# Kernel optimization log

Measured on AMD Instinct MI355X. Metric: run time of the kernel, lower is better.

Reference implementation:

```python
import jax, jax.numpy as jnp
import numpy as np

B = 262144
HID = 256
HEADS = 8


def setup_inputs() -> dict:
    key = jax.random.key(0)
    ks = jax.random.split(key, 8)
    s = 1.0 / np.sqrt(HID)
    return {
        "fine_messages": jax.random.normal(ks[0], (B, HID), jnp.float32),
        "coarse_messages": jax.random.normal(ks[1], (B, HID), jnp.float32),
        "motif_features": jax.random.normal(ks[2], (B, HID), jnp.float32),
        "Wq": jax.random.normal(ks[3], (HID, HID), jnp.float32) * s,
        "Wk": jax.random.normal(ks[4], (HID, HID), jnp.float32) * s,
        "Wv": jax.random.normal(ks[5], (HID, HID), jnp.float32) * s,
        "Wo": jax.random.normal(ks[6], (HID, HID), jnp.float32) * s,
        "bo": jax.random.normal(ks[7], (HID,), jnp.float32) * s,
        "heads": HEADS,
    }


def reference(fine_messages, coarse_messages, motif_features, Wq, Wk, Wv, Wo, bo, heads):
    b, hid = motif_features.shape
    d_k = hid // heads
    # K/V share the same pre-projection input: [fine; coarse] -> (B, 2, hid)
    kv_in = jnp.stack([fine_messages, coarse_messages], axis=1)
    # torch Linear(x) = x @ W.T (no bias on q/k/v projections)
    q = (motif_features @ Wq.T).reshape(b, heads, d_k)          # (B, H, d_k) single query
    k = (kv_in @ Wk.T).reshape(b, 2, heads, d_k)                # (B, 2, H, d_k)
    v = (kv_in @ Wv.T).reshape(b, 2, heads, d_k)
    # NOTE: original divides by d_k, not sqrt(d_k)
    scores = jnp.einsum("bhd,bshd->bhs", q, k) / d_k            # (B, H, 2)
    att = jax.nn.softmax(scores, axis=-1)
    out = jnp.einsum("bhs,bshd->bhd", att, v).reshape(b, hid)   # (B, hid)
    return out @ Wo.T + bo
```

## Files before the change

kernel.cpp:

```cpp
#include <hip/hip_runtime.h>

#define B_TOT 262144
#define HID   256
#define NHEAD 8
#define BR    64
#define NTHR  256

typedef __bf16 bf16_t;
typedef __attribute__((ext_vector_type(8))) __bf16 bf16x8;
typedef __attribute__((ext_vector_type(4))) float  f32x4;


#define PHASE_SYNC(N)                                                  \
  do {                                                                 \
    asm volatile("s_waitcnt vmcnt(" #N ") lgkmcnt(0)" ::: "memory");   \
    __builtin_amdgcn_s_barrier();                                      \
  } while (0)

static __device__ __forceinline__ f32x4 mfma16(bf16x8 a, bf16x8 b, f32x4 c) {
  return __builtin_amdgcn_mfma_f32_16x16x32_bf16(a, b, c, 0, 0, 0);
}

static __device__ __forceinline__ bf16x8 cvt8(float4 a, float4 b) {
  bf16x8 r;
  r[0] = (bf16_t)a.x; r[1] = (bf16_t)a.y; r[2] = (bf16_t)a.z; r[3] = (bf16_t)a.w;
  r[4] = (bf16_t)b.x; r[5] = (bf16_t)b.y; r[6] = (bf16_t)b.z; r[7] = (bf16_t)b.w;
  return r;
}

static __device__ __forceinline__ bf16x8 pin8(bf16x8 v) {
  f32x4 t = __builtin_bit_cast(f32x4, v);
  asm volatile("" : "+v"(t));
  return __builtin_bit_cast(bf16x8, t);
}

typedef __attribute__((address_space(3))) void lds_void;
typedef __attribute__((address_space(1))) void gbl_void;
static __device__ __forceinline__ void gload_lds16(const void* g, void* l) {
  __builtin_amdgcn_global_load_lds((gbl_void*)g, (lds_void*)l, 16, 0, 0);
}

__global__ __launch_bounds__(256) void pack_weights(
    const float* __restrict__ Wq, const float* __restrict__ Wk,
    const float* __restrict__ Wv, const float* __restrict__ Wo,
    bf16_t* __restrict__ ws) {
  const int t     = blockIdx.x * 256 + threadIdx.x;
  const int lane  = t & 63;
  const int chunk = t >> 6;
  const int l15 = lane & 15, lg = lane >> 4;
  const float* src;
  int row, col;
  if (chunk < 384) {
    const int ph = chunk >> 4;
    const int c  = chunk & 15;
    const int h = ph / 3, w = ph % 3;
    const int ks = c >> 1, half = c & 1;
    src = (w == 0) ? Wq : (w == 1) ? Wk : Wv;
    row = h * 32 + (l15 >> 2) * 8 + half * 4 + (l15 & 3);
    col = ks * 32 + lg * 8;
  } else {
    const int c  = chunk - 384;
    const int ks = c >> 4, jt = c & 15;
    src = Wo;
    row = jt * 16 + l15;
    col = ks * 32 + lg * 8;
  }
  const float* p = src + (size_t)row * HID + col;
  *(bf16x8*)(ws + (size_t)t * 8) = cvt8(*(const float4*)p, *(const float4*)(p + 4));
}

__global__ __launch_bounds__(NTHR, 2) void fused_local_aug(
    const float* __restrict__ fine, const float* __restrict__ coarse,
    const float* __restrict__ motif, const bf16_t* __restrict__ wpk,
    const float* __restrict__ bo, float* __restrict__ out) {
  __shared__ char wbuf[49152];

  const int tid  = threadIdx.x;
  const int lane = tid & 63;
  const int wave = tid >> 6;
  const int l15  = lane & 15;
  const int lg   = lane >> 4;
  const size_t mrow = (size_t)blockIdx.x * BR + wave * 16 + l15;

  auto stage = [&](int ph) {
    char* dst = wbuf + (ph % 3) * 16384 + tid * 16;
    const char* src = (const char*)wpk + (size_t)ph * 16384 + tid * 16;
#pragma unroll
    for (int i = 0; i < 4; ++i)
      gload_lds16(src + i * 4096, dst + i * 4096);
  };

  stage(0);
  stage(1);

  bf16x8 xm[8], xf[8], xc[8];
  {
    const float* pm = motif  + mrow * HID + lg * 8;
    const float* pf = fine   + mrow * HID + lg * 8;
    const float* pc = coarse + mrow * HID + lg * 8;
#pragma unroll
    for (int s = 0; s < 8; ++s) {
      xm[s] = pin8(cvt8(*(const float4*)(pm + s * 32), *(const float4*)(pm + s * 32 + 4)));
      xf[s] = pin8(cvt8(*(const float4*)(pf + s * 32), *(const float4*)(pf + s * 32 + 4)));
      xc[s] = pin8(cvt8(*(const float4*)(pc + s * 32), *(const float4*)(pc + s * 32 + 4)));
    }
  }
  __syncthreads();

  bf16x8 mfrag[NHEAD];
  const f32x4 z4 = {0.f, 0.f, 0.f, 0.f};

  f32x4 aQ0[2], aQ1[2], aK10[2], aK11[2], aK20[2], aK21[2],
        aV10[2], aV11[2], aV20[2], aV21[2];

#pragma unroll
  for (int h = 0; h < NHEAD; ++h) {
    const int cur = h & 1, prv = cur ^ 1;
    {
      const int p = 3 * h;
      if (p > 0) PHASE_SYNC(4);
      stage(p + 2);
      aQ0[cur] = z4; aQ1[cur] = z4;
      const char* pb = wbuf + (p % 3) * 16384 + lane * 16;
      __builtin_amdgcn_s_setprio(1);
#pragma unroll
      for (int ks = 0; ks < 8; ++ks) {
        bf16x8 q0 = *(const bf16x8*)(pb + ks * 2048);
        bf16x8 q1 = *(const bf16x8*)(pb + ks * 2048 + 1024);
        aQ0[cur] = mfma16(q0, xm[ks], aQ0[cur]);
        aQ1[cur] = mfma16(q1, xm[ks], aQ1[cur]);
      }
      __builtin_amdgcn_s_setprio(0);
      if (h > 0) {
        float s1 = 0.f, s2 = 0.f;
#pragma unroll
        for (int r = 0; r < 4; ++r) {
          s1 += aQ0[prv][r] * aK10[prv][r] + aQ1[prv][r] * aK11[prv][r];
          s2 += aQ0[prv][r] * aK20[prv][r] + aQ1[prv][r] * aK21[prv][r];
        }
        s1 += __shfl_xor(s1, 16); s1 += __shfl_xor(s1, 32);
        s2 += __shfl_xor(s2, 16); s2 += __shfl_xor(s2, 32);
        s1 *= (1.0f / 32.0f);  s2 *= (1.0f / 32.0f);
        const float mx = fmaxf(s1, s2);
        const float e1 = __expf(s1 - mx), e2 = __expf(s2 - mx);
        const float a1 = e1 / (e1 + e2);
        const float a2 = 1.0f - a1;
        bf16x8 t;
#pragma unroll
        for (int r = 0; r < 4; ++r) {
          t[r]     = (bf16_t)(a1 * aV10[prv][r] + a2 * aV20[prv][r]);
          t[r + 4] = (bf16_t)(a1 * aV11[prv][r] + a2 * aV21[prv][r]);
        }
        mfrag[h - 1] = t;
      }
    }
    {
      const int p = 3 * h + 1;
      PHASE_SYNC(4);
      stage(p + 2);
      aK10[cur] = z4; aK11[cur] = z4; aK20[cur] = z4; aK21[cur] = z4;
      const char* pb = wbuf + (p % 3) * 16384 + lane * 16;
      __builtin_amdgcn_s_setprio(1);
#pragma unroll
      for (int ks = 0; ks < 8; ++ks) {
        bf16x8 k0 = *(const bf16x8*)(pb + ks * 2048);
        bf16x8 k1 = *(const bf16x8*)(pb + ks * 2048 + 1024);
        aK10[cur] = mfma16(k0, xf[ks], aK10[cur]);
        aK11[cur] = mfma16(k1, xf[ks], aK11[cur]);
        aK20[cur] = mfma16(k0, xc[ks], aK20[cur]);
        aK21[cur] = mfma16(k1, xc[ks], aK21[cur]);
      }
      __builtin_amdgcn_s_setprio(0);
    }
    {
      const int p = 3 * h + 2;
      PHASE_SYNC(4);
      stage(p + 2);
      aV10[cur] = z4; aV11[cur] = z4; aV20[cur] = z4; aV21[cur] = z4;
      const char* pb = wbuf + (p % 3) * 16384 + lane * 16;
      __builtin_amdgcn_s_setprio(1);
#pragma unroll
      for (int ks = 0; ks < 8; ++ks) {
        bf16x8 v0 = *(const bf16x8*)(pb + ks * 2048);
        bf16x8 v1 = *(const bf16x8*)(pb + ks * 2048 + 1024);
        aV10[cur] = mfma16(v0, xf[ks], aV10[cur]);
        aV11[cur] = mfma16(v1, xf[ks], aV11[cur]);
        aV20[cur] = mfma16(v0, xc[ks], aV20[cur]);
        aV21[cur] = mfma16(v1, xc[ks], aV21[cur]);
      }
      __builtin_amdgcn_s_setprio(0);
    }
  }
  {
    const int prv = 1;
    float s1 = 0.f, s2 = 0.f;
#pragma unroll
    for (int r = 0; r < 4; ++r) {
      s1 += aQ0[prv][r] * aK10[prv][r] + aQ1[prv][r] * aK11[prv][r];
      s2 += aQ0[prv][r] * aK20[prv][r] + aQ1[prv][r] * aK21[prv][r];
    }
    s1 += __shfl_xor(s1, 16); s1 += __shfl_xor(s1, 32);
    s2 += __shfl_xor(s2, 16); s2 += __shfl_xor(s2, 32);
    s1 *= (1.0f / 32.0f);  s2 *= (1.0f / 32.0f);
    const float mx = fmaxf(s1, s2);
    const float e1 = __expf(s1 - mx), e2 = __expf(s2 - mx);
    const float a1 = e1 / (e1 + e2);
    const float a2 = 1.0f - a1;
    bf16x8 t;
#pragma unroll
    for (int r = 0; r < 4; ++r) {
      t[r]     = (bf16_t)(a1 * aV10[prv][r] + a2 * aV20[prv][r]);
      t[r + 4] = (bf16_t)(a1 * aV11[prv][r] + a2 * aV21[prv][r]);
    }
    mfrag[NHEAD - 1] = t;
  }

  f32x4 acc[16];
#pragma unroll
  for (int jt = 0; jt < 16; ++jt) acc[jt] = z4;

#pragma unroll
  for (int wp = 0; wp < 8; ++wp) {
    const int p = 24 + wp;
    if (wp == 7) { PHASE_SYNC(0); } else { PHASE_SYNC(4); }
    if (wp < 6) stage(p + 2);
    bf16x8 m = mfrag[wp];
    const char* pb = wbuf + (p % 3) * 16384 + lane * 16;
    __builtin_amdgcn_s_setprio(1);
#pragma unroll
    for (int jt = 0; jt < 16; ++jt) {
      bf16x8 wf = *(const bf16x8*)(pb + jt * 1024);
      acc[jt] = mfma16(wf, m, acc[jt]);
    }
    __builtin_amdgcn_s_setprio(0);
  }

#pragma unroll
  for (int jt = 0; jt < 16; ++jt) {
    const int jj = jt * 16 + lg * 4;
    const float4 b4 = *(const float4*)(bo + jj);
    f32x4 o;
    o[0] = acc[jt][0] + b4.x;
    o[1] = acc[jt][1] + b4.y;
    o[2] = acc[jt][2] + b4.z;
    o[3] = acc[jt][3] + b4.w;
    __builtin_nontemporal_store(o, (f32x4*)(out + mrow * HID + jj));
  }
}

extern "C" void kernel_launch(void* const* d_in, const int* in_sizes, int n_in,
                              void* d_out, int out_size, void* d_ws, size_t ws_size,
                              hipStream_t stream) {
  (void)in_sizes; (void)n_in; (void)ws_size; (void)out_size;
  const float* fine   = (const float*)d_in[0];
  const float* coarse = (const float*)d_in[1];
  const float* motif  = (const float*)d_in[2];
  const float* Wq     = (const float*)d_in[3];
  const float* Wk     = (const float*)d_in[4];
  const float* Wv     = (const float*)d_in[5];
  const float* Wo     = (const float*)d_in[6];
  const float* bo     = (const float*)d_in[7];
  float* out          = (float*)d_out;
  bf16_t* wpk         = (bf16_t*)d_ws;

  pack_weights<<<128, 256, 0, stream>>>(Wq, Wk, Wv, Wo, wpk);
  fused_local_aug<<<B_TOT / BR, NTHR, 0, stream>>>(fine, coarse, motif, wpk, bo, out);
}
```

Measured before the change: 344.6 us.

## Give each wave two 16-row tiles to reuse LDS weight fragments

The block shrinks from four waves to two, and each wave now handles 32 rows as two 16-row sub-tiles. Every weight fragment read from LDS therefore feeds two MFMAs instead of one, halving LDS read traffic per row. The score dot products are also computed right after the V phase instead of being deferred through double-buffered accumulators. The cost is about twice the registers per wave (inputs and the 32 output accumulators), occupancy is relaxed to one block per launch bound, and each thread now issues twice as many weight-staging loads with a deeper wait count.

Measured after the change: 495.0 us. +43.6%, slower.

```diff
diff --git a/kernel.cpp b/kernel.cpp
--- a/kernel.cpp
+++ b/kernel.cpp
@@ -4,7 +4,7 @@
 #define HID   256
 #define NHEAD 8
 #define BR    64
-#define NTHR  256
+#define NTHR  128
 
 typedef __bf16 bf16_t;
 typedef __attribute__((ext_vector_type(8))) __bf16 bf16x8;
@@ -69,7 +69,7 @@
   *(bf16x8*)(ws + (size_t)t * 8) = cvt8(*(const float4*)p, *(const float4*)(p + 4));
 }
 
-__global__ __launch_bounds__(NTHR, 2) void fused_local_aug(
+__global__ __launch_bounds__(NTHR, 1) void fused_local_aug(
     const float* __restrict__ fine, const float* __restrict__ coarse,
     const float* __restrict__ motif, const bf16_t* __restrict__ wpk,
     const float* __restrict__ bo, float* __restrict__ out) {
@@ -80,157 +80,179 @@
   const int wave = tid >> 6;
   const int l15  = lane & 15;
   const int lg   = lane >> 4;
-  const size_t mrow = (size_t)blockIdx.x * BR + wave * 16 + l15;
+  const size_t rowb = (size_t)blockIdx.x * BR + wave * 32 + l15;
 
   auto stage = [&](int ph) {
     char* dst = wbuf + (ph % 3) * 16384 + tid * 16;
     const char* src = (const char*)wpk + (size_t)ph * 16384 + tid * 16;
 #pragma unroll
-    for (int i = 0; i < 4; ++i)
-      gload_lds16(src + i * 4096, dst + i * 4096);
+    for (int i = 0; i < 8; ++i)
+      gload_lds16(src + i * 2048, dst + i * 2048);
   };
 
   stage(0);
   stage(1);
 
-  bf16x8 xm[8], xf[8], xc[8];
-  {
-    const float* pm = motif  + mrow * HID + lg * 8;
-    const float* pf = fine   + mrow * HID + lg * 8;
-    const float* pc = coarse + mrow * HID + lg * 8;
+  bf16x8 xm[2][8], xf[2][8], xc[2][8];
+#pragma unroll
+  for (int t = 0; t < 2; ++t) {
+    const size_t r = rowb + t * 16;
+    const float* pm = motif  + r * HID + lg * 8;
+    const float* pf = fine   + r * HID + lg * 8;
+    const float* pc = coarse + r * HID + lg * 8;
 #pragma unroll
     for (int s = 0; s < 8; ++s) {
-      xm[s] = pin8(cvt8(*(const float4*)(pm + s * 32), *(const float4*)(pm + s * 32 + 4)));
-      xf[s] = pin8(cvt8(*(const float4*)(pf + s * 32), *(const float4*)(pf + s * 32 + 4)));
-      xc[s] = pin8(cvt8(*(const float4*)(pc + s * 32), *(const float4*)(pc + s * 32 + 4)));
+      xm[t][s] = pin8(cvt8(*(const float4*)(pm + s * 32), *(const float4*)(pm + s * 32 + 4)));
+      xf[t][s] = pin8(cvt8(*(const float4*)(pf + s * 32), *(const float4*)(pf + s * 32 + 4)));
+      xc[t][s] = pin8(cvt8(*(const float4*)(pc + s * 32), *(const float4*)(pc + s * 32 + 4)));
     }
   }
   __syncthreads();
 
-  bf16x8 mfrag[NHEAD];
+  bf16x8 mfrag[NHEAD][2];
   const f32x4 z4 = {0.f, 0.f, 0.f, 0.f};
 
-  f32x4 aQ0[2], aQ1[2], aK10[2], aK11[2], aK20[2], aK21[2],
-        aV10[2], aV11[2], aV20[2], aV21[2];
+  f32x4 aQ[2][2], aK1[2][2], aK2[2][2], aV1[2][2], aV2[2][2];
+  float ps1[2], ps2[2];
 
 #pragma unroll
   for (int h = 0; h < NHEAD; ++h) {
-    const int cur = h & 1, prv = cur ^ 1;
     {
       const int p = 3 * h;
-      if (p > 0) PHASE_SYNC(4);
+      if (p > 0) PHASE_SYNC(8);
       stage(p + 2);
-      aQ0[cur] = z4; aQ1[cur] = z4;
+#pragma unroll
+      for (int t = 0; t < 2; ++t) { aQ[0][t] = z4; aQ[1][t] = z4; }
       const char* pb = wbuf + (p % 3) * 16384 + lane * 16;
       __builtin_amdgcn_s_setprio(1);
 #pragma unroll
       for (int ks = 0; ks < 8; ++ks) {
         bf16x8 q0 = *(const bf16x8*)(pb + ks * 2048);
         bf16x8 q1 = *(const bf16x8*)(pb + ks * 2048 + 1024);
-        aQ0[cur] = mfma16(q0, xm[ks], aQ0[cur]);
-        aQ1[cur] = mfma16(q1, xm[ks], aQ1[cur]);
+#pragma unroll
+        for (int t = 0; t < 2; ++t) {
+          aQ[0][t] = mfma16(q0, xm[t][ks], aQ[0][t]);
+          aQ[1][t] = mfma16(q1, xm[t][ks], aQ[1][t]);
+        }
       }
       __builtin_amdgcn_s_setprio(0);
       if (h > 0) {
-        float s1 = 0.f, s2 = 0.f;
-#pragma unroll
-        for (int r = 0; r < 4; ++r) {
-          s1 += aQ0[prv][r] * aK10[prv][r] + aQ1[prv][r] * aK11[prv][r];
-          s2 += aQ0[prv][r] * aK20[prv][r] + aQ1[prv][r] * aK21[prv][r];
-        }
-        s1 += __shfl_xor(s1, 16); s1 += __shfl_xor(s1, 32);
-        s2 += __shfl_xor(s2, 16); s2 += __shfl_xor(s2, 32);
-        s1 *= (1.0f / 32.0f);  s2 *= (1.0f / 32.0f);
-        const float mx = fmaxf(s1, s2);
-        const float e1 = __expf(s1 - mx), e2 = __expf(s2 - mx);
-        const float a1 = e1 / (e1 + e2);
-        const float a2 = 1.0f - a1;
-        bf16x8 t;
-#pragma unroll
-        for (int r = 0; r < 4; ++r) {
-          t[r]     = (bf16_t)(a1 * aV10[prv][r] + a2 * aV20[prv][r]);
-          t[r + 4] = (bf16_t)(a1 * aV11[prv][r] + a2 * aV21[prv][r]);
-        }
-        mfrag[h - 1] = t;
+#pragma unroll
+        for (int t = 0; t < 2; ++t) {
+          float s1 = ps1[t], s2 = ps2[t];
+          s1 += __shfl_xor(s1, 16); s1 += __shfl_xor(s1, 32);
+          s2 += __shfl_xor(s2, 16); s2 += __shfl_xor(s2, 32);
+          s1 *= (1.0f / 32.0f);  s2 *= (1.0f / 32.0f);
+          const float mx = fmaxf(s1, s2);
+          const float e1 = __expf(s1 - mx), e2 = __expf(s2 - mx);
+          const float a1 = e1 / (e1 + e2);
+          const float a2 = 1.0f - a1;
+          bf16x8 m;
+#pragma unroll
+          for (int r = 0; r < 4; ++r) {
+            m[r]     = (bf16_t)(a1 * aV1[0][t][r] + a2 * aV2[0][t][r]);
+            m[r + 4] = (bf16_t)(a1 * aV1[1][t][r] + a2 * aV2[1][t][r]);
+          }
+          mfrag[h - 1][t] = m;
+        }
       }
     }
     {
       const int p = 3 * h + 1;
-      PHASE_SYNC(4);
+      PHASE_SYNC(8);
       stage(p + 2);
-      aK10[cur] = z4; aK11[cur] = z4; aK20[cur] = z4; aK21[cur] = z4;
+#pragma unroll
+      for (int t = 0; t < 2; ++t) {
+        aK1[0][t] = z4; aK1[1][t] = z4; aK2[0][t] = z4; aK2[1][t] = z4;
+      }
       const char* pb = wbuf + (p % 3) * 16384 + lane * 16;
       __builtin_amdgcn_s_setprio(1);
 #pragma unroll
       for (int ks = 0; ks < 8; ++ks) {
         bf16x8 k0 = *(const bf16x8*)(pb + ks * 2048);
         bf16x8 k1 = *(const bf16x8*)(pb + ks * 2048 + 1024);
-        aK10[cur] = mfma16(k0, xf[ks], aK10[cur]);
-        aK11[cur] = mfma16(k1, xf[ks], aK11[cur]);
-        aK20[cur] = mfma16(k0, xc[ks], aK20[cur]);
-        aK21[cur] = mfma16(k1, xc[ks], aK21[cur]);
+#pragma unroll
+        for (int t = 0; t < 2; ++t) {
+          aK1[0][t] = mfma16(k0, xf[t][ks], aK1[0][t]);
+          aK1[1][t] = mfma16(k1, xf[t][ks], aK1[1][t]);
+          aK2[0][t] = mfma16(k0, xc[t][ks], aK2[0][t]);
+          aK2[1][t] = mfma16(k1, xc[t][ks], aK2[1][t]);
+        }
       }
       __builtin_amdgcn_s_setprio(0);
     }
     {
       const int p = 3 * h + 2;
-      PHASE_SYNC(4);
+      PHASE_SYNC(8);
       stage(p + 2);
-      aV10[cur] = z4; aV11[cur] = z4; aV20[cur] = z4; aV21[cur] = z4;
+#pragma unroll
+      for (int t = 0; t < 2; ++t) {
+        aV1[0][t] = z4; aV1[1][t] = z4; aV2[0][t] = z4; aV2[1][t] = z4;
+      }
       const char* pb = wbuf + (p % 3) * 16384 + lane * 16;
       __builtin_amdgcn_s_setprio(1);
 #pragma unroll
       for (int ks = 0; ks < 8; ++ks) {
         bf16x8 v0 = *(const bf16x8*)(pb + ks * 2048);
         bf16x8 v1 = *(const bf16x8*)(pb + ks * 2048 + 1024);
-        aV10[cur] = mfma16(v0, xf[ks], aV10[cur]);
-        aV11[cur] = mfma16(v1, xf[ks], aV11[cur]);
-        aV20[cur] = mfma16(v0, xc[ks], aV20[cur]);
-        aV21[cur] = mfma16(v1, xc[ks], aV21[cur]);
+#pragma unroll
+        for (int t = 0; t < 2; ++t) {
+          aV1[0][t] = mfma16(v0, xf[t][ks], aV1[0][t]);
+          aV1[1][t] = mfma16(v1, xf[t][ks], aV1[1][t]);
+          aV2[0][t] = mfma16(v0, xc[t][ks], aV2[0][t]);
+          aV2[1][t] = mfma16(v1, xc[t][ks], aV2[1][t]);
+        }
       }
       __builtin_amdgcn_s_setprio(0);
+#pragma unroll
+      for (int t = 0; t < 2; ++t) {
+        float s1 = 0.f, s2 = 0.f;
+#pragma unroll
+        for (int r = 0; r < 4; ++r) {
+          s1 += aQ[0][t][r] * aK1[0][t][r] + aQ[1][t][r] * aK1[1][t][r];
+          s2 += aQ[0][t][r] * aK2[0][t][r] + aQ[1][t][r] * aK2[1][t][r];
+        }
+        ps1[t] = s1; ps2[t] = s2;
+      }
     }
   }
   {
-    const int prv = 1;
-    float s1 = 0.f, s2 = 0.f;
-#pragma unroll
-    for (int r = 0; r < 4; ++r) {
-      s1 += aQ0[prv][r] * aK10[prv][r] + aQ1[prv][r] * aK11[prv][r];
-      s2 += aQ0[prv][r] * aK20[prv][r] + aQ1[prv][r] * aK21[prv][r];
-    }
-    s1 += __shfl_xor(s1, 16); s1 += __shfl_xor(s1, 32);
-    s2 += __shfl_xor(s2, 16); s2 += __shfl_xor(s2, 32);
-    s1 *= (1.0f / 32.0f);  s2 *= (1.0f / 32.0f);
-    const float mx = fmaxf(s1, s2);
-    const float e1 = __expf(s1 - mx), e2 = __expf(s2 - mx);
-    const float a1 = e1 / (e1 + e2);
-    const float a2 = 1.0f - a1;
-    bf16x8 t;
-#pragma unroll
-    for (int r = 0; r < 4; ++r) {
-      t[r]     = (bf16_t)(a1 * aV10[prv][r] + a2 * aV20[prv][r]);
-      t[r + 4] = (bf16_t)(a1 * aV11[prv][r] + a2 * aV21[prv][r]);
-    }
-    mfrag[NHEAD - 1] = t;
-  }
-
-  f32x4 acc[16];
-#pragma unroll
-  for (int jt = 0; jt < 16; ++jt) acc[jt] = z4;
+#pragma unroll
+    for (int t = 0; t < 2; ++t) {
+      float s1 = ps1[t], s2 = ps2[t];
+      s1 += __shfl_xor(s1, 16); s1 += __shfl_xor(s1, 32);
+      s2 += __shfl_xor(s2, 16); s2 += __shfl_xor(s2, 32);
+      s1 *= (1.0f / 32.0f);  s2 *= (1.0f / 32.0f);
+      const float mx = fmaxf(s1, s2);
+      const float e1 = __expf(s1 - mx), e2 = __expf(s2 - mx);
+      const float a1 = e1 / (e1 + e2);
+      const float a2 = 1.0f - a1;
+      bf16x8 m;
+#pragma unroll
+      for (int r = 0; r < 4; ++r) {
+        m[r]     = (bf16_t)(a1 * aV1[0][t][r] + a2 * aV2[0][t][r]);
+        m[r + 4] = (bf16_t)(a1 * aV1[1][t][r] + a2 * aV2[1][t][r]);
+      }
+      mfrag[NHEAD - 1][t] = m;
+    }
+  }
+
+  f32x4 acc[16][2];
+#pragma unroll
+  for (int jt = 0; jt < 16; ++jt) { acc[jt][0] = z4; acc[jt][1] = z4; }
 
 #pragma unroll
   for (int wp = 0; wp < 8; ++wp) {
     const int p = 24 + wp;
-    if (wp == 7) { PHASE_SYNC(0); } else { PHASE_SYNC(4); }
+    if (wp == 7) { PHASE_SYNC(0); } else { PHASE_SYNC(8); }
     if (wp < 6) stage(p + 2);
-    bf16x8 m = mfrag[wp];
     const char* pb = wbuf + (p % 3) * 16384 + lane * 16;
     __builtin_amdgcn_s_setprio(1);
 #pragma unroll
     for (int jt = 0; jt < 16; ++jt) {
       bf16x8 wf = *(const bf16x8*)(pb + jt * 1024);
-      acc[jt] = mfma16(wf, m, acc[jt]);
+      acc[jt][0] = mfma16(wf, mfrag[wp][0], acc[jt][0]);
+      acc[jt][1] = mfma16(wf, mfrag[wp][1], acc[jt][1]);
     }
     __builtin_amdgcn_s_setprio(0);
   }
@@ -239,12 +261,15 @@
   for (int jt = 0; jt < 16; ++jt) {
     const int jj = jt * 16 + lg * 4;
     const float4 b4 = *(const float4*)(bo + jj);
-    f32x4 o;
-    o[0] = acc[jt][0] + b4.x;
-    o[1] = acc[jt][1] + b4.y;
-    o[2] = acc[jt][2] + b4.z;
-    o[3] = acc[jt][3] + b4.w;
-    __builtin_nontemporal_store(o, (f32x4*)(out + mrow * HID + jj));
+#pragma unroll
+    for (int t = 0; t < 2; ++t) {
+      f32x4 o;
+      o[0] = acc[jt][t][0] + b4.x;
+      o[1] = acc[jt][t][1] + b4.y;
+      o[2] = acc[jt][t][2] + b4.z;
+      o[3] = acc[jt][t][3] + b4.w;
+      __builtin_nontemporal_store(o, (f32x4*)(out + (rowb + t * 16) * HID + jj));
+    }
   }
 }
 
```
